# Performance work log

Measured on AMD Instinct MI355X. Metric: run time of the kernel, lower is better.

## Reference

```python
import jax, jax.numpy as jnp
import numpy as np

D_ENC, D_PRED, D_JOINT, VOCAB = 512, 640, 640, 1024
LOGIT_CLAMP = 15.0


def setup_inputs() -> dict:
    key = jax.random.key(0)
    ks = jax.random.split(key, 8)
    B, T, U = 4, 256, 64
    enc = jax.random.normal(ks[0], (B, T, D_ENC), dtype=jnp.float32)
    pred = jax.random.normal(ks[1], (B, U, D_PRED), dtype=jnp.float32)
    s_e = 1.0 / np.sqrt(D_ENC)
    s_p = 1.0 / np.sqrt(D_PRED)
    s_j = 1.0 / np.sqrt(D_JOINT)
    W_enc = jax.random.uniform(ks[2], (D_ENC, D_JOINT), jnp.float32, -s_e, s_e)
    b_enc = jax.random.uniform(ks[3], (D_JOINT,), jnp.float32, -s_e, s_e)
    W_pred = jax.random.uniform(ks[4], (D_PRED, D_JOINT), jnp.float32, -s_p, s_p)
    b_pred = jax.random.uniform(ks[5], (D_JOINT,), jnp.float32, -s_p, s_p)
    W_out = jax.random.uniform(ks[6], (D_JOINT, VOCAB), jnp.float32, -s_j, s_j)
    b_out = jax.random.uniform(ks[7], (VOCAB,), jnp.float32, -s_j, s_j)
    return {"encoder_out": enc, "predictor_out": pred,
            "W_enc": W_enc, "b_enc": b_enc,
            "W_pred": W_pred, "b_pred": b_pred,
            "W_out": W_out, "b_out": b_out}


def reference(encoder_out, predictor_out, W_enc, b_enc, W_pred, b_pred, W_out, b_out):
    # (B,T,d_joint) and (B,U,d_joint) projections
    enc = jnp.einsum('bte,ej->btj', encoder_out, W_enc) + b_enc
    pred = jnp.einsum('bup,pj->buj', predictor_out, W_pred) + b_pred
    # broadcast add -> (B,T,U,d_joint), tanh, vocab projection
    joint = jnp.tanh(enc[:, :, None, :] + pred[:, None, :, :])
    logits = jnp.einsum('btuj,jv->btuv', joint, W_out) + b_out
    return jnp.clip(logits, -LOGIT_CLAMP, LOGIT_CLAMP)
```

## Files before the change

kernel.cpp:

```cpp
#include <hip/hip_runtime.h>

typedef unsigned short u16;
typedef unsigned int u32;
typedef __bf16 bf16x8 __attribute__((ext_vector_type(8)));
typedef float f32x4 __attribute__((ext_vector_type(4)));

#define T_DIM 256
#define U_DIM 64
#define DJ 640
#define VOCAB 1024

typedef __attribute__((address_space(3))) u32 lds_u32;
typedef const __attribute__((address_space(1))) u32 glb_u32;

__device__ __forceinline__ u16 f2bf(float f) {
    u32 x = __float_as_uint(f);
    x += 0x7fffu + ((x >> 16) & 1u);
    return (u16)(x >> 16);
}

__device__ __forceinline__ float fast_tanh(float x) {
    float e = __expf(2.0f * x);
    return 1.0f - 2.0f / (e + 1.0f);
}

__global__ __launch_bounds__(128) void prep_kernel(const float* __restrict__ enc,
                                                   const float* __restrict__ W_enc,
                                                   const float* __restrict__ b_enc,
                                                   const float* __restrict__ pred,
                                                   const float* __restrict__ W_pred,
                                                   const float* __restrict__ b_pred,
                                                   const float* __restrict__ W_out,
                                                   float* __restrict__ enc_proj,
                                                   float* __restrict__ pred_proj,
                                                   u16* __restrict__ Wt) {
    __shared__ float smem[4 * 640];
    int b = blockIdx.x;
    int tid = threadIdx.x;

    if (b < 1600) {
        const float* X; const float* W; const float* bias; float* out; int K, r0, jj;
        if (b < 1280) {
            X = enc;  W = W_enc;  bias = b_enc;  out = enc_proj;  K = 512;
            r0 = (b & 255) * 4;  jj = (b >> 8) * 128 + tid;
        } else {
            int b2 = b - 1280;
            X = pred; W = W_pred; bias = b_pred; out = pred_proj; K = 640;
            r0 = (b2 & 63) * 4;  jj = (b2 >> 6) * 128 + tid;
        }
        float* xs = smem;
        for (int idx = tid; idx < 4 * K; idx += 128) {
            int r = idx / K, k = idx - r * K;
            xs[r * K + k] = X[(size_t)(r0 + r) * K + k];
        }
        __syncthreads();
        float bb = bias[jj];
        float a0 = bb, a1 = bb, a2 = bb, a3 = bb;
#pragma unroll 8
        for (int k = 0; k < K; k++) {
            float w = W[(size_t)k * DJ + jj];
            a0 = fmaf(xs[k], w, a0);
            a1 = fmaf(xs[K + k], w, a1);
            a2 = fmaf(xs[2 * K + k], w, a2);
            a3 = fmaf(xs[3 * K + k], w, a3);
        }
        out[(size_t)(r0 + 0) * DJ + jj] = a0;
        out[(size_t)(r0 + 1) * DJ + jj] = a1;
        out[(size_t)(r0 + 2) * DJ + jj] = a2;
        out[(size_t)(r0 + 3) * DJ + jj] = a3;
    } else {
        float (*tile)[33] = (float(*)[33])smem;
        int b3 = b - 1600;
        int n0 = (b3 & 31) * 32, k0 = (b3 >> 5) * 32;
        int tx = tid & 31, ty4 = tid >> 5;
#pragma unroll
        for (int j = 0; j < 8; j++)
            tile[ty4 + j * 4][tx] = W_out[(size_t)(k0 + ty4 + j * 4) * VOCAB + n0 + tx];
        __syncthreads();
#pragma unroll
        for (int j = 0; j < 8; j++)
            Wt[(size_t)(n0 + ty4 + j * 4) * DJ + k0 + tx] = f2bf(tile[tx][ty4 + j * 4]);
    }
}

__global__ __launch_bounds__(256) void tanh_kernel(const float* __restrict__ encp,
                                                   const float* __restrict__ predp,
                                                   u16* __restrict__ A) {
    int id = blockIdx.x * 256 + threadIdx.x;
    int m = id / 80;
    int c = id - m * 80;
    int koff = c * 8;
    int b = m >> 14, t = (m >> 6) & 255, u = m & 63;
    const float4* pe = (const float4*)(encp + (size_t)(b * T_DIM + t) * DJ + koff);
    const float4* pp = (const float4*)(predp + (size_t)(b * U_DIM + u) * DJ + koff);
    float4 e0 = pe[0], e1 = pe[1];
    float4 p0 = pp[0], p1 = pp[1];
    uint4 v;
    v.x = (u32)f2bf(fast_tanh(e0.x + p0.x)) | ((u32)f2bf(fast_tanh(e0.y + p0.y)) << 16);
    v.y = (u32)f2bf(fast_tanh(e0.z + p0.z)) | ((u32)f2bf(fast_tanh(e0.w + p0.w)) << 16);
    v.z = (u32)f2bf(fast_tanh(e1.x + p1.x)) | ((u32)f2bf(fast_tanh(e1.y + p1.y)) << 16);
    v.w = (u32)f2bf(fast_tanh(e1.z + p1.z)) | ((u32)f2bf(fast_tanh(e1.w + p1.w)) << 16);
    *(uint4*)(A + (size_t)id * 8) = v;
}

__global__ __launch_bounds__(256) void gemm_kernel(const u16* __restrict__ A,
                                                   const u16* __restrict__ Wt,
                                                   const float* __restrict__ b_out,
                                                   float* __restrict__ out) {
    __shared__ u16 smem[2 * 128 * 64];
    u16* As = smem;
    u16* Bs = smem + 128 * 64;

    int bid = blockIdx.x;
    int swz = (bid & 7) * 512 + (bid >> 3);
    int ntile = swz & 7;
    int mtile = swz >> 3;
    int row0 = mtile * 128;
    int n0 = ntile * 128;

    int tid = threadIdx.x;
    int lane = tid & 63;
    int wave = tid >> 6;
    int wm = wave & 1;
    int wn = wave >> 1;
    int lm = lane & 15;
    int quad = lane >> 4;

    int rS = wave * 8 + (lane >> 3);
    int kSwz = ((lane ^ (lane >> 3)) & 7) * 8;
    const u16* gA = A + (size_t)(row0 + rS) * DJ + kSwz;
    const u16* gB = Wt + (size_t)(n0 + rS) * DJ + kSwz;
    u16* lA = As + wave * 8 * 64;
    u16* lB = Bs + wave * 8 * 64;

    int abase = (wm * 64 + lm) * 64;
    int bbase = (wn * 64 + lm) * 64;
    int c0 = ((quad ^ (lm & 7))) * 8;
    int c1 = (((quad ^ 4) ^ (lm & 7))) * 8;

    f32x4 acc[4][4];
#pragma unroll
    for (int i = 0; i < 4; i++)
#pragma unroll
        for (int j = 0; j < 4; j++) {
            acc[i][j][0] = 0.f; acc[i][j][1] = 0.f;
            acc[i][j][2] = 0.f; acc[i][j][3] = 0.f;
        }

    for (int k0 = 0; k0 < DJ; k0 += 64) {
#pragma unroll
        for (int i = 0; i < 4; i++) {
            __builtin_amdgcn_global_load_lds((glb_u32*)(gA + (size_t)i * 32 * DJ + k0),
                                             (lds_u32*)(lA + i * 32 * 64), 16, 0, 0);
            __builtin_amdgcn_global_load_lds((glb_u32*)(gB + (size_t)i * 32 * DJ + k0),
                                             (lds_u32*)(lB + i * 32 * 64), 16, 0, 0);
        }
        __syncthreads();

        bf16x8 af[4], bfr[4];
#pragma unroll
        for (int i = 0; i < 4; i++)
            af[i] = *(const bf16x8*)(As + abase + i * 16 * 64 + c0);
#pragma unroll
        for (int j = 0; j < 4; j++)
            bfr[j] = *(const bf16x8*)(Bs + bbase + j * 16 * 64 + c0);
#pragma unroll
        for (int i = 0; i < 4; i++)
#pragma unroll
            for (int j = 0; j < 4; j++)
                acc[i][j] = __builtin_amdgcn_mfma_f32_16x16x32_bf16(af[i], bfr[j], acc[i][j], 0, 0, 0);
#pragma unroll
        for (int i = 0; i < 4; i++)
            af[i] = *(const bf16x8*)(As + abase + i * 16 * 64 + c1);
#pragma unroll
        for (int j = 0; j < 4; j++)
            bfr[j] = *(const bf16x8*)(Bs + bbase + j * 16 * 64 + c1);
#pragma unroll
        for (int i = 0; i < 4; i++)
#pragma unroll
            for (int j = 0; j < 4; j++)
                acc[i][j] = __builtin_amdgcn_mfma_f32_16x16x32_bf16(af[i], bfr[j], acc[i][j], 0, 0, 0);

        __syncthreads();
    }

    float* cs = (float*)smem;
#pragma unroll
    for (int rnd = 0; rnd < 2; rnd++) {
        __syncthreads();
#pragma unroll
        for (int ii = 0; ii < 2; ii++) {
            int i = rnd * 2 + ii;
            int lrow = wm * 32 + ii * 16 + quad * 4;
#pragma unroll
            for (int j = 0; j < 4; j++) {
                int lcol = wn * 64 + j * 16 + lm;
#pragma unroll
                for (int r = 0; r < 4; r++)
                    cs[(lrow + r) * 128 + lcol] = acc[i][j][r];
            }
        }
        __syncthreads();
#pragma unroll
        for (int t = 0; t < 8; t++) {
            int g = tid + t * 256;
            int lrow2 = g >> 5;
            int gc4 = (g & 31) * 4;
            f32x4 v = *(const f32x4*)(cs + lrow2 * 128 + gc4);
            f32x4 b4 = *(const f32x4*)(b_out + n0 + gc4);
            int grow = row0 + (lrow2 >> 5) * 64 + rnd * 32 + (lrow2 & 31);
#pragma unroll
            for (int cc = 0; cc < 4; cc++) {
                float x = v[cc] + b4[cc];
                v[cc] = fminf(fmaxf(x, -15.0f), 15.0f);
            }
            *(f32x4*)(out + (size_t)grow * VOCAB + n0 + gc4) = v;
        }
    }
}

#define LDA 40
__global__ __launch_bounds__(256) void joint_fused(const float* __restrict__ encp,
                                                   const float* __restrict__ predp,
                                                   const u16* __restrict__ Wt,
                                                   const float* __restrict__ b_out,
                                                   float* __restrict__ out) {
    __shared__ u16 As[128 * LDA];
    __shared__ u16 Bs[128 * LDA];
    int ntile = blockIdx.x & 7;
    int mtile = blockIdx.x >> 3;
    int row0 = mtile * 128;
    int bidx = row0 >> 14;
    int t0 = (row0 & 16383) >> 6;
    int n0 = ntile * 128;
    int tid = threadIdx.x, lane = tid & 63, wave = tid >> 6;
    int wm = wave & 1, wn = wave >> 1, lm = lane & 15, quad = lane >> 4;
    int am = tid >> 1, ak = (tid & 1) << 4;
    const float* encA = encp + (size_t)(bidx * T_DIM + t0 + (am >> 6)) * DJ + ak;
    const float* predA = predp + (size_t)(bidx * U_DIM + (am & 63)) * DJ + ak;
    u16* Asw = As + am * LDA + ak;
    int bn = tid >> 1, bk = (tid & 1) << 4;
    const u16* WtB = Wt + (size_t)(n0 + bn) * DJ + bk;
    u16* Bsw = Bs + bn * LDA + bk;
    f32x4 acc[4][4];
#pragma unroll
    for (int i = 0; i < 4; i++)
#pragma unroll
        for (int j = 0; j < 4; j++) {
            acc[i][j][0] = 0.f; acc[i][j][1] = 0.f; acc[i][j][2] = 0.f; acc[i][j][3] = 0.f;
        }
    for (int k0 = 0; k0 < DJ; k0 += 32) {
        const float4* pe = (const float4*)(encA + k0);
        const float4* pp = (const float4*)(predA + k0);
#pragma unroll
        for (int i = 0; i < 4; i++) {
            float4 e = pe[i]; float4 p = pp[i];
            uint2 v;
            v.x = (u32)f2bf(fast_tanh(e.x + p.x)) | ((u32)f2bf(fast_tanh(e.y + p.y)) << 16);
            v.y = (u32)f2bf(fast_tanh(e.z + p.z)) | ((u32)f2bf(fast_tanh(e.w + p.w)) << 16);
            *(uint2*)(Asw + i * 4) = v;
        }
        const u16* src = WtB + k0;
        uint4 w0 = *(const uint4*)src;
        uint4 w1 = *(const uint4*)(src + 8);
        *(uint4*)Bsw = w0;
        *(uint4*)(Bsw + 8) = w1;
        __syncthreads();
        bf16x8 af[4], bfr[4];
#pragma unroll
        for (int i = 0; i < 4; i++)
            af[i] = *(const bf16x8*)(As + (wm * 64 + i * 16 + lm) * LDA + quad * 8);
#pragma unroll
        for (int j = 0; j < 4; j++)
            bfr[j] = *(const bf16x8*)(Bs + (wn * 64 + j * 16 + lm) * LDA + quad * 8);
#pragma unroll
        for (int i = 0; i < 4; i++)
#pragma unroll
            for (int j = 0; j < 4; j++)
                acc[i][j] = __builtin_amdgcn_mfma_f32_16x16x32_bf16(af[i], bfr[j], acc[i][j], 0, 0, 0);
        __syncthreads();
    }
#pragma unroll
    for (int j = 0; j < 4; j++) {
        int gc = n0 + wn * 64 + j * 16 + lm;
        float bo = b_out[gc];
#pragma unroll
        for (int i = 0; i < 4; i++) {
            int gr = row0 + wm * 64 + i * 16 + quad * 4;
#pragma unroll
            for (int r = 0; r < 4; r++) {
                float v = acc[i][j][r] + bo;
                v = fminf(fmaxf(v, -15.0f), 15.0f);
                out[(size_t)(gr + r) * VOCAB + gc] = v;
            }
        }
    }
}

extern "C" void kernel_launch(void* const* d_in, const int* in_sizes, int n_in,
                              void* d_out, int out_size, void* d_ws, size_t ws_size,
                              hipStream_t stream) {
    const float* enc    = (const float*)d_in[0];
    const float* pred   = (const float*)d_in[1];
    const float* W_enc  = (const float*)d_in[2];
    const float* b_enc  = (const float*)d_in[3];
    const float* W_pred = (const float*)d_in[4];
    const float* b_pred = (const float*)d_in[5];
    const float* W_out  = (const float*)d_in[6];
    const float* b_out  = (const float*)d_in[7];
    float* out = (float*)d_out;

    float* enc_proj  = (float*)d_ws;
    float* pred_proj = enc_proj + 1024 * DJ;
    u16*   Wt        = (u16*)(pred_proj + 256 * DJ);
    u16*   Abuf      = Wt + 1024 * DJ;

    size_t need = (size_t)(1024 + 256) * DJ * 4 + (size_t)1024 * DJ * 2
                + (size_t)65536 * DJ * 2;

    prep_kernel<<<dim3(2240), dim3(128), 0, stream>>>(enc, W_enc, b_enc,
                                                      pred, W_pred, b_pred,
                                                      W_out, enc_proj, pred_proj, Wt);

    if (ws_size >= need) {
        tanh_kernel<<<dim3(65536 * 80 / 256), dim3(256), 0, stream>>>(enc_proj, pred_proj, Abuf);
        gemm_kernel<<<dim3(4096), dim3(256), 0, stream>>>(Abuf, Wt, b_out, out);
    } else {
        joint_fused<<<dim3(4096), dim3(256), 0, stream>>>(enc_proj, pred_proj, Wt, b_out, out);
    }
}
```

Measured before the change: 432.7 us.

## Rewrite GEMM as 256x256 tile, 8-wave kernel with double-buffered LDS pipeline

Replaces the 128x128, 4-wave GEMM with a 256x256 tile computed by 8 waves. The kernel double-buffers LDS across K tiles split into halves, interleaving async global-to-LDS loads with MFMA blocks. It uses barriers, s_setprio and manual vmcnt waits to keep loads in flight during compute. The goal is higher data reuse per tile and hiding global-load latency behind MFMA work, at the cost of more LDS and registers (launch_bounds 512,2) and complex synchronization.

```diff
diff --git a/kernel.cpp b/kernel.cpp
--- a/kernel.cpp
+++ b/kernel.cpp
@@ -103,118 +103,178 @@
     *(uint4*)(A + (size_t)id * 8) = v;
 }
 
-__global__ __launch_bounds__(256) void gemm_kernel(const u16* __restrict__ A,
-                                                   const u16* __restrict__ Wt,
-                                                   const float* __restrict__ b_out,
-                                                   float* __restrict__ out) {
-    __shared__ u16 smem[2 * 128 * 64];
-    u16* As = smem;
-    u16* Bs = smem + 128 * 64;
+__global__ __launch_bounds__(512, 2) void gemm_kernel(const u16* __restrict__ A,
+                                                      const u16* __restrict__ Wt,
+                                                      const float* __restrict__ b_out,
+                                                      float* __restrict__ out) {
+    __shared__ u16 lds[2][2][2][8192];
 
     int bid = blockIdx.x;
-    int swz = (bid & 7) * 512 + (bid >> 3);
-    int ntile = swz & 7;
-    int mtile = swz >> 3;
-    int row0 = mtile * 128;
-    int n0 = ntile * 128;
+    int swz = (bid & 7) * 128 + (bid >> 3);
+    int ntile = swz & 3;
+    int mtile = swz >> 2;
+    int row0 = mtile * 256;
+    int n0 = ntile * 256;
 
     int tid = threadIdx.x;
     int lane = tid & 63;
     int wave = tid >> 6;
     int wm = wave & 1;
-    int wn = wave >> 1;
+    int wn_ = wave >> 1;
     int lm = lane & 15;
     int quad = lane >> 4;
 
-    int rS = wave * 8 + (lane >> 3);
-    int kSwz = ((lane ^ (lane >> 3)) & 7) * 8;
-    const u16* gA = A + (size_t)(row0 + rS) * DJ + kSwz;
-    const u16* gB = Wt + (size_t)(n0 + rS) * DJ + kSwz;
-    u16* lA = As + wave * 8 * 64;
-    u16* lB = Bs + wave * 8 * 64;
-
-    int abase = (wm * 64 + lm) * 64;
-    int bbase = (wn * 64 + lm) * 64;
-    int c0 = ((quad ^ (lm & 7))) * 8;
-    int c1 = (((quad ^ 4) ^ (lm & 7))) * 8;
-
-    f32x4 acc[4][4];
-#pragma unroll
-    for (int i = 0; i < 4; i++)
-#pragma unroll
-        for (int j = 0; j < 4; j++) {
-            acc[i][j][0] = 0.f; acc[i][j][1] = 0.f;
-            acc[i][j][2] = 0.f; acc[i][j][3] = 0.f;
-        }
-
-    for (int k0 = 0; k0 < DJ; k0 += 64) {
-#pragma unroll
-        for (int i = 0; i < 4; i++) {
-            __builtin_amdgcn_global_load_lds((glb_u32*)(gA + (size_t)i * 32 * DJ + k0),
-                                             (lds_u32*)(lA + i * 32 * 64), 16, 0, 0);
-            __builtin_amdgcn_global_load_lds((glb_u32*)(gB + (size_t)i * 32 * DJ + k0),
-                                             (lds_u32*)(lB + i * 32 * 64), 16, 0, 0);
-        }
-        __syncthreads();
-
-        bf16x8 af[4], bfr[4];
-#pragma unroll
-        for (int i = 0; i < 4; i++)
-            af[i] = *(const bf16x8*)(As + abase + i * 16 * 64 + c0);
-#pragma unroll
-        for (int j = 0; j < 4; j++)
-            bfr[j] = *(const bf16x8*)(Bs + bbase + j * 16 * 64 + c0);
-#pragma unroll
-        for (int i = 0; i < 4; i++)
-#pragma unroll
-            for (int j = 0; j < 4; j++)
-                acc[i][j] = __builtin_amdgcn_mfma_f32_16x16x32_bf16(af[i], bfr[j], acc[i][j], 0, 0, 0);
-#pragma unroll
-        for (int i = 0; i < 4; i++)
-            af[i] = *(const bf16x8*)(As + abase + i * 16 * 64 + c1);
-#pragma unroll
-        for (int j = 0; j < 4; j++)
-            bfr[j] = *(const bf16x8*)(Bs + bbase + j * 16 * 64 + c1);
-#pragma unroll
-        for (int i = 0; i < 4; i++)
-#pragma unroll
-            for (int j = 0; j < 4; j++)
-                acc[i][j] = __builtin_amdgcn_mfma_f32_16x16x32_bf16(af[i], bfr[j], acc[i][j], 0, 0, 0);
-
-        __syncthreads();
-    }
-
-    float* cs = (float*)smem;
+    auto stage = [&](int buf, int mat, int kt, int kh) {
+#pragma unroll
+        for (int j = 0; j < 2; j++) {
+            int sidx = tid + j * 512;
+            int r = sidx >> 2;
+            int c = (sidx & 3) ^ (r & 3);
+            const u16* src = mat ? (Wt + (size_t)(n0 + r) * DJ)
+                                 : (A + (size_t)(row0 + r) * DJ);
+            __builtin_amdgcn_global_load_lds(
+                (glb_u32*)(src + kt * 64 + kh * 32 + c * 8),
+                (lds_u32*)(&lds[buf][mat][kh][(wave * 64 + j * 512) * 8]), 16, 0, 0);
+        }
+    };
+    auto rdA = [&](int buf, int kh, int f) -> bf16x8 {
+        int row = wm * 128 + f * 16 + lm;
+        return *(const bf16x8*)(&lds[buf][0][kh][row * 32 + ((quad ^ (lm & 3)) * 8)]);
+    };
+    auto rdB = [&](int buf, int kh, int g) -> bf16x8 {
+        int row = wn_ * 64 + g * 16 + lm;
+        return *(const bf16x8*)(&lds[buf][1][kh][row * 32 + ((quad ^ (lm & 3)) * 8)]);
+    };
+
+    f32x4 acc[8][4];
+#pragma unroll
+    for (int m = 0; m < 8; m++)
+#pragma unroll
+        for (int n = 0; n < 4; n++) {
+            acc[m][n][0] = 0.f; acc[m][n][1] = 0.f;
+            acc[m][n][2] = 0.f; acc[m][n][3] = 0.f;
+        }
+
+#define MFMA_QUAD(MLO, AF, BF)                                                        \
+    _Pragma("unroll") for (int m = 0; m < 4; m++)                                     \
+    _Pragma("unroll") for (int n = 0; n < 4; n++)                                     \
+        acc[(MLO) + m][n] = __builtin_amdgcn_mfma_f32_16x16x32_bf16(                  \
+            AF[(MLO) + m], BF[n], acc[(MLO) + m][n], 0, 0, 0);
+
+    stage(0, 0, 0, 0); stage(0, 1, 0, 0); stage(0, 0, 0, 1); stage(0, 1, 0, 1);
+    stage(1, 0, 1, 0); stage(1, 1, 1, 0); stage(1, 0, 1, 1);
+    asm volatile("s_waitcnt vmcnt(6)" ::: "memory");
+    __builtin_amdgcn_s_barrier();
+
+    for (int i = 0; i < 5; ++i) {
+        int t2 = 2 * i + 2, t3 = 2 * i + 3;
+        bool more = (i < 4);
+        bf16x8 a0[8], a1[8], b0[4], b1[4];
+
+#pragma unroll
+        for (int f = 0; f < 8; f++) a0[f] = rdA(0, 0, f);
+#pragma unroll
+        for (int g = 0; g < 4; g++) b0[g] = rdB(0, 0, g);
+        stage(1, 1, 2 * i + 1, 1);
+        __builtin_amdgcn_s_barrier();
+        __builtin_amdgcn_s_setprio(1);
+        MFMA_QUAD(0, a0, b0)
+        __builtin_amdgcn_s_setprio(0);
+        __builtin_amdgcn_s_barrier();
+
+#pragma unroll
+        for (int f = 0; f < 8; f++) a1[f] = rdA(0, 1, f);
+        if (more) stage(0, 0, t2, 0);
+        __builtin_amdgcn_s_barrier();
+        __builtin_amdgcn_s_setprio(1);
+        MFMA_QUAD(4, a0, b0)
+        __builtin_amdgcn_s_setprio(0);
+        __builtin_amdgcn_s_barrier();
+
+#pragma unroll
+        for (int g = 0; g < 4; g++) b1[g] = rdB(0, 1, g);
+        if (more) stage(0, 1, t2, 0);
+        __builtin_amdgcn_s_barrier();
+        __builtin_amdgcn_s_setprio(1);
+        MFMA_QUAD(0, a1, b1)
+        __builtin_amdgcn_s_setprio(0);
+        __builtin_amdgcn_s_barrier();
+
+        if (more) stage(0, 0, t2, 1);
+        __builtin_amdgcn_s_barrier();
+        __builtin_amdgcn_s_setprio(1);
+        MFMA_QUAD(4, a1, b1)
+        __builtin_amdgcn_s_setprio(0);
+        if (more) { asm volatile("s_waitcnt vmcnt(6)" ::: "memory"); }
+        else      { asm volatile("s_waitcnt vmcnt(0)" ::: "memory"); }
+        __builtin_amdgcn_s_barrier();
+
+#pragma unroll
+        for (int f = 0; f < 8; f++) a0[f] = rdA(1, 0, f);
+#pragma unroll
+        for (int g = 0; g < 4; g++) b0[g] = rdB(1, 0, g);
+        if (more) stage(0, 1, t2, 1);
+        __builtin_amdgcn_s_barrier();
+        __builtin_amdgcn_s_setprio(1);
+        MFMA_QUAD(0, a0, b0)
+        __builtin_amdgcn_s_setprio(0);
+        __builtin_amdgcn_s_barrier();
+
+#pragma unroll
+        for (int f = 0; f < 8; f++) a1[f] = rdA(1, 1, f);
+        if (more) stage(1, 0, t3, 0);
+        __builtin_amdgcn_s_barrier();
+        __builtin_amdgcn_s_setprio(1);
+        MFMA_QUAD(4, a0, b0)
+        __builtin_amdgcn_s_setprio(0);
+        __builtin_amdgcn_s_barrier();
+
+#pragma unroll
+        for (int g = 0; g < 4; g++) b1[g] = rdB(1, 1, g);
+        if (more) stage(1, 1, t3, 0);
+        __builtin_amdgcn_s_barrier();
+        __builtin_amdgcn_s_setprio(1);
+        MFMA_QUAD(0, a1, b1)
+        __builtin_amdgcn_s_setprio(0);
+        __builtin_amdgcn_s_barrier();
+
+        if (more) stage(1, 0, t3, 1);
+        __builtin_amdgcn_s_barrier();
+        __builtin_amdgcn_s_setprio(1);
+        MFMA_QUAD(4, a1, b1)
+        __builtin_amdgcn_s_setprio(0);
+        if (more) { asm volatile("s_waitcnt vmcnt(6)" ::: "memory"); }
+        __builtin_amdgcn_s_barrier();
+    }
+#undef MFMA_QUAD
+
+    float* cs = (float*)lds;
 #pragma unroll
     for (int rnd = 0; rnd < 2; rnd++) {
         __syncthreads();
-#pragma unroll
-        for (int ii = 0; ii < 2; ii++) {
-            int i = rnd * 2 + ii;
-            int lrow = wm * 32 + ii * 16 + quad * 4;
-#pragma unroll
-            for (int j = 0; j < 4; j++) {
-                int lcol = wn * 64 + j * 16 + lm;
-#pragma unroll
-                for (int r = 0; r < 4; r++)
-                    cs[(lrow + r) * 128 + lcol] = acc[i][j][r];
-            }
-        }
-        __syncthreads();
-#pragma unroll
-        for (int t = 0; t < 8; t++) {
-            int g = tid + t * 256;
-            int lrow2 = g >> 5;
-            int gc4 = (g & 31) * 4;
-            f32x4 v = *(const f32x4*)(cs + lrow2 * 128 + gc4);
-            f32x4 b4 = *(const f32x4*)(b_out + n0 + gc4);
-            int grow = row0 + (lrow2 >> 5) * 64 + rnd * 32 + (lrow2 & 31);
+        if (wm == rnd) {
+#pragma unroll
+            for (int m = 0; m < 8; m++)
+#pragma unroll
+                for (int j = 0; j < 4; j++)
+#pragma unroll
+                    for (int r = 0; r < 4; r++)
+                        cs[(m * 16 + quad * 4 + r) * 256 + wn_ * 64 + j * 16 + lm] = acc[m][j][r];
+        }
+        __syncthreads();
+#pragma unroll
+        for (int p = 0; p < 16; p++) {
+            int g = tid + p * 512;
+            int rw = g >> 6;
+            int c4 = (g & 63) * 4;
+            f32x4 v = *(const f32x4*)(cs + rw * 256 + c4);
+            f32x4 b4 = *(const f32x4*)(b_out + n0 + c4);
 #pragma unroll
             for (int cc = 0; cc < 4; cc++) {
                 float x = v[cc] + b4[cc];
                 v[cc] = fminf(fmaxf(x, -15.0f), 15.0f);
             }
-            *(f32x4*)(out + (size_t)grow * VOCAB + n0 + gc4) = v;
+            *(f32x4*)(out + (size_t)(row0 + rnd * 128 + rw) * VOCAB + n0 + c4) = v;
         }
     }
 }
@@ -324,7 +384,7 @@
 
     if (ws_size >= need) {
         tanh_kernel<<<dim3(65536 * 80 / 256), dim3(256), 0, stream>>>(enc_proj, pred_proj, Abuf);
-        gemm_kernel<<<dim3(4096), dim3(256), 0, stream>>>(Abuf, Wt, b_out, out);
+        gemm_kernel<<<dim3(1024), dim3(512), 0, stream>>>(Abuf, Wt, b_out, out);
     } else {
         joint_fused<<<dim3(4096), dim3(256), 0, stream>>>(enc_proj, pred_proj, Wt, b_out, out);
     }
```

Result: no change. 433.6 us (+0.2%).
